# Performance work log

Measured on AMD Instinct MI355X. Metric: run time of the kernel, lower is better.

Reference implementation:

```python
import jax, jax.numpy as jnp
import numpy as np

UNITS = 768
OUT_STEPS = 64
INPUT_DIM = 96


def setup_inputs() -> dict:
    key = jax.random.key(0)
    ks = jax.random.split(key, 7)
    B, T = 2048, 24
    s_ih = 1.0 / np.sqrt(UNITS)
    inputs = jax.random.normal(ks[0], (B, T, INPUT_DIM), dtype=jnp.float32)
    # PyTorch LSTMCell params: weight_ih [4U, I], weight_hh [4U, U], biases [4U]
    W_ih = jax.random.uniform(ks[1], (4 * UNITS, INPUT_DIM), minval=-s_ih, maxval=s_ih, dtype=jnp.float32)
    W_hh = jax.random.uniform(ks[2], (4 * UNITS, UNITS), minval=-s_ih, maxval=s_ih, dtype=jnp.float32)
    b_ih = jax.random.uniform(ks[3], (4 * UNITS,), minval=-s_ih, maxval=s_ih, dtype=jnp.float32)
    b_hh = jax.random.uniform(ks[4], (4 * UNITS,), minval=-s_ih, maxval=s_ih, dtype=jnp.float32)
    # Dense: Linear(units, input_dim)
    s_d = 1.0 / np.sqrt(UNITS)
    W_d = jax.random.uniform(ks[5], (INPUT_DIM, UNITS), minval=-s_d, maxval=s_d, dtype=jnp.float32)
    b_d = jax.random.uniform(ks[6], (INPUT_DIM,), minval=-s_d, maxval=s_d, dtype=jnp.float32)
    return {"inputs": inputs, "W_ih": W_ih, "W_hh": W_hh, "b_ih": b_ih, "b_hh": b_hh, "W_d": W_d, "b_d": b_d}


def _lstm_cell(x, h, c, W_ih, W_hh, b_ih, b_hh):
    # gates: [B, 4U], PyTorch gate order i, f, g, o
    gates = x @ W_ih.T + b_ih + h @ W_hh.T + b_hh
    i, f, g, o = jnp.split(gates, 4, axis=-1)
    i = jax.nn.sigmoid(i)
    f = jax.nn.sigmoid(f)
    g = jnp.tanh(g)
    o = jax.nn.sigmoid(o)
    c_new = f * c + i * g
    h_new = o * jnp.tanh(c_new)
    return h_new, c_new


def reference(inputs, W_ih, W_hh, b_ih, b_hh, W_d, b_d):
    B = inputs.shape[0]
    h0 = jnp.zeros((B, UNITS), dtype=inputs.dtype)
    c0 = jnp.zeros((B, UNITS), dtype=inputs.dtype)
    # warmup: feed last timestep
    x0 = inputs[:, -1, :]
    h, c = _lstm_cell(x0, h0, c0, W_ih, W_hh, b_ih, b_hh)
    pred0 = h @ W_d.T + b_d

    def step(carry, _):
        pred, h, c = carry
        h2, c2 = _lstm_cell(pred, h, c, W_ih, W_hh, b_ih, b_hh)
        pred2 = h2 @ W_d.T + b_d
        return (pred2, h2, c2), pred2

    _, preds_rest = jax.lax.scan(step, (pred0, h, c), None, length=OUT_STEPS - 1)
    # preds_rest: [out_steps-1, B, I] -> stack with pred0 along time axis 1
    preds = jnp.concatenate([pred0[None], preds_rest], axis=0)  # [out_steps, B, I]
    return jnp.transpose(preds, (1, 0, 2))  # [B, out_steps, I]
```

## Files before the change

kernel.cpp:

```cpp
#include <hip/hip_runtime.h>
#include <hip/hip_bf16.h>
#include <stdint.h>

typedef __hip_bfloat16 bf16_t;
typedef __attribute__((ext_vector_type(4))) float f32x4;
typedef __attribute__((ext_vector_type(8))) short s16x8;

#define UNITS 768
#define NCOLS 3072
#define NPRED 96
#define MROWS 2048

__device__ __forceinline__ float sigf(float x) {
    return __builtin_amdgcn_rcpf(1.f + __expf(-x));
}
__device__ __forceinline__ float tanh_fast(float x) {
    return 1.f - 2.f * __builtin_amdgcn_rcpf(1.f + __expf(2.f * x));
}


__global__ void prep_b0(const float* __restrict__ W_ih, bf16_t* __restrict__ B0T) {
    int idx = blockIdx.x * 256 + threadIdx.x;
    if (idx >= NCOLS * 96) return;
    int c = idx / 96, k = idx % 96;
    int u = ((c >> 6) << 4) + (c & 15);
    int g = (c >> 4) & 3;
    B0T[idx] = (bf16_t)W_ih[(g * UNITS + u) * 96 + k];
}

__global__ void prep_x0(const float* __restrict__ inputs, bf16_t* __restrict__ x0) {
    int idx = blockIdx.x * 256 + threadIdx.x;
    int j = idx & 7;
    int l = (idx >> 3) & 63;
    int fg = idx >> 9;
    int kf = fg % 3;
    int mf = fg / 3;
    int m = mf * 16 + (l & 15);
    int k = kf * 32 + (l >> 4) * 8 + j;
    x0[idx] = (bf16_t)inputs[(m * 24 + 23) * 96 + k];
}

__global__ void prep_bias(const float* __restrict__ b_ih, const float* __restrict__ b_hh,
                          const float* __restrict__ W_ih, const float* __restrict__ b_d,
                          float* __restrict__ b0_r, float* __restrict__ beff_r) {
    int c = blockIdx.x * 256 + threadIdx.x;
    if (c >= NCOLS) return;
    int u = ((c >> 6) << 4) + (c & 15);
    int g = (c >> 4) & 3;
    int r = g * UNITS + u;
    float v = b_ih[r] + b_hh[r];
    float acc = 0.f;
    for (int j = 0; j < 96; ++j) acc += W_ih[r * 96 + j] * b_d[j];
    b0_r[c] = v;
    beff_r[c] = v + acc;
}

__global__ void prep_beff2(const float* __restrict__ W_hh, const float* __restrict__ W_ih,
                           const float* __restrict__ W_d, bf16_t* __restrict__ BeffT) {
    __shared__ float sWih[64][96];
    __shared__ float sWd[96][64];
    const int c0 = blockIdx.x * 64, k0 = blockIdx.y * 64;
    const int tid = threadIdx.x;
    for (int i = tid; i < 64 * 96; i += 256) {
        int cc = i / 96, j = i % 96;
        int c = c0 + cc;
        int u = ((c >> 6) << 4) + (c & 15);
        int g = (c >> 4) & 3;
        sWih[cc][j] = W_ih[(g * UNITS + u) * 96 + j];
    }
    for (int i = tid; i < 96 * 64; i += 256) {
        int j = i / 64, kk = i % 64;
        sWd[j][kk] = W_d[j * UNITS + k0 + kk];
    }
    __syncthreads();
    const int kk = tid & 63;
    const int cc0 = (tid >> 6) * 16;
    for (int cc = cc0; cc < cc0 + 16; ++cc) {
        float acc = 0.f;
#pragma unroll 12
        for (int j = 0; j < 96; ++j) acc += sWih[cc][j] * sWd[j][kk];
        int c = c0 + cc;
        int u = ((c >> 6) << 4) + (c & 15);
        int g = (c >> 4) & 3;
        int r = g * UNITS + u;
        BeffT[(size_t)c * UNITS + k0 + kk] = (bf16_t)(W_hh[(size_t)r * UNITS + k0 + kk] + acc);
    }
}

__global__ void prep_wdt(const float* __restrict__ W_d, bf16_t* __restrict__ BeffT) {
    int idx = blockIdx.x * 256 + threadIdx.x;
    int c = idx / UNITS, k = idx % UNITS;
    float v = (c < NPRED) ? W_d[c * UNITS + k] : 0.f;
    BeffT[(size_t)(NCOLS + c) * UNITS + k] = (bf16_t)v;
}

__global__ void prep_swz(const bf16_t* __restrict__ src, bf16_t* __restrict__ dst,
                         int Knk, int K, int total) {
    int idx = blockIdx.x * 256 + threadIdx.x;
    if (idx >= total) return;
    int j = idx & 7;
    int l = (idx >> 3) & 63;
    int fg = idx >> 9;
    int f = fg & 3;
    int rest = fg >> 2;
    int kf = rest % Knk;
    int nw = rest / Knk;
    int c = (nw >> 1) * 128 + (nw & 1) * 64 + f * 16 + (l & 15);
    int k = kf * 32 + (l >> 4) * 8 + j;
    dst[idx] = src[(size_t)c * K + k];
}

__global__ __launch_bounds__(256, 2)
void step_kernel(const bf16_t* __restrict__ A,
                 const bf16_t* __restrict__ B,
                 const float* __restrict__ bias_r,
                 const float* __restrict__ b_d,
                 float* __restrict__ c_state,
                 bf16_t* __restrict__ h_out,
                 float* __restrict__ out,
                 int Knk, int nt_off, int t, int is_first)
{
    const int tid = threadIdx.x;
    const int wave = tid >> 6;
    const int lane = tid & 63;
    const int wr = wave >> 1, wc = wave & 1;
    const int l15 = lane & 15, l4 = lane >> 4;

    const int per = gridDim.x >> 3;
    const int g = (blockIdx.x & 7) * per + (blockIdx.x >> 3);
    const int nt = nt_off + (g >> 4);
    const int mt = g & 15;
    const int n0 = nt * 128;
    const bool is_pred = (nt >= 24);

    const bf16_t* Ab[4];
#pragma unroll
    for (int i = 0; i < 4; ++i)
        Ab[i] = A + ((size_t)((mt * 8 + wr * 4 + i) * Knk) * 64 + lane) * 8;
    const bf16_t* Bb[4];
#pragma unroll
    for (int f = 0; f < 4; ++f)
        Bb[f] = B + ((size_t)((nt * 2 + wc) * Knk * 4 + f) * 64 + lane) * 8;

    const int u = nt * 32 + wc * 16 + l15;
    const int slot = nt * 16 + mt;
    float* cbase = c_state + (((size_t)slot * 4 + wave) * 64 + lane) * 16;
    f32x4 cold4[4];
    float bi[4];
#pragma unroll
    for (int q = 0; q < 4; ++q) cold4[q] = f32x4{0.f, 0.f, 0.f, 0.f};
    if (!is_pred) {
        if (!is_first) {
#pragma unroll
            for (int q = 0; q < 4; ++q) cold4[q] = *(const f32x4*)(cbase + q * 4);
        }
#pragma unroll
        for (int f = 0; f < 4; ++f) bi[f] = bias_r[n0 + wc * 64 + f * 16 + l15];
    } else {
#pragma unroll
        for (int f = 0; f < 4; ++f) {
            int j = wc * 64 + f * 16 + l15;
            bi[f] = (j < NPRED) ? b_d[j] : 0.f;
        }
    }

    f32x4 acc[4][4];
#pragma unroll
    for (int i = 0; i < 4; ++i)
#pragma unroll
        for (int j = 0; j < 4; ++j) acc[i][j] = f32x4{0.f, 0.f, 0.f, 0.f};

    s16x8 afr[3][4], bfr[3][4];
    const int nk = Knk;

#define LOADK(BUF, KT) do {                                                          \
        _Pragma("unroll")                                                            \
        for (int _i = 0; _i < 4; ++_i)                                               \
            afr[BUF][_i] = *(const s16x8*)(Ab[_i] + (size_t)(KT) * 512);             \
        _Pragma("unroll")                                                            \
        for (int _f = 0; _f < 4; ++_f)                                               \
            bfr[BUF][_f] = *(const s16x8*)(Bb[_f] + (size_t)(KT) * 2048);            \
    } while (0)
#define MF(BUF) do {                                                                 \
        _Pragma("unroll")                                                            \
        for (int _i = 0; _i < 4; ++_i)                                               \
            _Pragma("unroll")                                                        \
            for (int _j = 0; _j < 4; ++_j)                                           \
                acc[_i][_j] = __builtin_amdgcn_mfma_f32_16x16x32_bf16(               \
                    afr[BUF][_i], bfr[BUF][_j], acc[_i][_j], 0, 0, 0);               \
    } while (0)

    LOADK(0, 0);
    LOADK(1, 1);
    const int nk3 = nk / 3;
    for (int b3 = 0; b3 < nk3; ++b3) {
        const int kt = b3 * 3;
        if (kt + 2 < nk) LOADK(2, kt + 2);
        MF(0);
        if (kt + 3 < nk) LOADK(0, kt + 3);
        MF(1);
        if (kt + 4 < nk) LOADK(1, kt + 4);
        MF(2);
    }
#undef LOADK
#undef MF

    if (!is_pred) {
        const int kq = wc * 2 + (l15 >> 3);
        const int jj = l15 & 7;
        f32x4 cnew4[4];
#pragma unroll
        for (int i = 0; i < 4; ++i) {
            const int mf = mt * 8 + wr * 4 + i;
            bf16_t* hb = h_out + (size_t)(mf * 24 + nt) * 512;
#pragma unroll
            for (int r = 0; r < 4; ++r) {
                float gi = acc[i][0][r] + bi[0];
                float gf = acc[i][1][r] + bi[1];
                float gg = acc[i][2][r] + bi[2];
                float go = acc[i][3][r] + bi[3];
                float si = sigf(gi);
                float sf = sigf(gf);
                float tg = tanh_fast(gg);
                float so = sigf(go);
                float cn = sf * cold4[i][r] + si * tg;
                cnew4[i][r] = cn;
                int lp = (l4 * 4 + r) | (kq << 4);
                hb[lp * 8 + jj] = (bf16_t)(so * tanh_fast(cn));
            }
        }
#pragma unroll
        for (int q = 0; q < 4; ++q) *(f32x4*)(cbase + q * 4) = cnew4[q];
    } else {
#pragma unroll
        for (int f = 0; f < 4; ++f) {
            int j = wc * 64 + f * 16 + l15;
            if (j < NPRED) {
#pragma unroll
                for (int i = 0; i < 4; ++i)
#pragma unroll
                    for (int r = 0; r < 4; ++r) {
                        int row = mt * 128 + wr * 64 + i * 16 + l4 * 4 + r;
                        out[((size_t)row * 64 + (t - 1)) * NPRED + j] = acc[i][f][r] + bi[f];
                    }
            }
        }
    }
}

extern "C" void kernel_launch(void* const* d_in, const int* in_sizes, int n_in,
                              void* d_out, int out_size, void* d_ws, size_t ws_size,
                              hipStream_t stream)
{
    const float* inputs = (const float*)d_in[0];
    const float* W_ih   = (const float*)d_in[1];
    const float* W_hh   = (const float*)d_in[2];
    const float* b_ih   = (const float*)d_in[3];
    const float* b_hh   = (const float*)d_in[4];
    const float* W_d    = (const float*)d_in[5];
    const float* b_d    = (const float*)d_in[6];
    float* out = (float*)d_out;

    char* ws = (char*)d_ws;
    size_t off = 0;
    auto alloc = [&](size_t bytes) -> char* {
        char* p = ws + off;
        off = (off + bytes + 255) & ~(size_t)255;
        return p;
    };
    bf16_t* B0T   = (bf16_t*)alloc((size_t)NCOLS * 96 * 2);
    bf16_t* B0s   = (bf16_t*)alloc((size_t)NCOLS * 96 * 2);
    bf16_t* BeffT = (bf16_t*)alloc((size_t)3200 * UNITS * 2);
    bf16_t* Bs    = (bf16_t*)alloc((size_t)3200 * UNITS * 2);
    bf16_t* x0s   = (bf16_t*)alloc((size_t)MROWS * 96 * 2);
    bf16_t* h0    = (bf16_t*)alloc((size_t)MROWS * UNITS * 2);
    bf16_t* h1    = (bf16_t*)alloc((size_t)MROWS * UNITS * 2);
    float*  cst   = (float*)alloc((size_t)384 * 4 * 64 * 16 * 4);
    float*  b0r   = (float*)alloc(NCOLS * 4);
    float*  beffr = (float*)alloc(NCOLS * 4);

    prep_b0   <<<(NCOLS * 96 + 255) / 256, 256, 0, stream>>>(W_ih, B0T);
    prep_swz  <<<(NCOLS * 96 + 255) / 256, 256, 0, stream>>>(B0T, B0s, 3, 96, NCOLS * 96);
    prep_x0   <<<(MROWS * 96) / 256, 256, 0, stream>>>(inputs, x0s);
    prep_bias <<<(NCOLS + 255) / 256, 256, 0, stream>>>(b_ih, b_hh, W_ih, b_d, b0r, beffr);
    prep_beff2<<<dim3(48, 12), 256, 0, stream>>>(W_hh, W_ih, W_d, BeffT);
    prep_wdt  <<<(128 * UNITS) / 256, 256, 0, stream>>>(W_d, BeffT);
    prep_swz  <<<(3200 * UNITS + 255) / 256, 256, 0, stream>>>(BeffT, Bs, 24, UNITS, 3200 * UNITS);

    bf16_t* h[2] = {h0, h1};

    step_kernel<<<384, 256, 0, stream>>>(x0s, B0s, b0r, b_d, cst, h[1], out, 3, 0, 0, 1);
    for (int n = 1; n < 64; ++n)
        step_kernel<<<400, 256, 0, stream>>>(h[n & 1], Bs, beffr, b_d, cst,
                                             h[(n + 1) & 1], out, 24, 0, n, 0);
    step_kernel<<<16, 256, 0, stream>>>(h[0], Bs, beffr, b_d, cst, h[1], out,
                                        24, 24, 64, 0);
    (void)ws_size; (void)in_sizes; (void)n_in; (void)out_size;
}
```

Baseline: 1.347 ms.

## Replace per-step launches with persistent LSTM kernel using LDS-resident weights

Replaces the 65 per-timestep launches with one persistent kernel of 200 blocks. Each block keeps its 64-column weight slice in shared memory for all steps, keeps the cell state in registers, and synchronises with the other blocks of its row group through atomic counters in global memory. This removes launch overhead, repeated weight reloads from global memory, and cell-state round trips. In exchange it relies on all 200 blocks being co-resident and adds a spin barrier with a timeout escape after every step.

```diff
diff --git a/kernel.cpp b/kernel.cpp
--- a/kernel.cpp
+++ b/kernel.cpp
@@ -110,77 +110,108 @@
     dst[idx] = src[(size_t)c * K + k];
 }
 
-__global__ __launch_bounds__(256, 2)
-void step_kernel(const bf16_t* __restrict__ A,
-                 const bf16_t* __restrict__ B,
-                 const float* __restrict__ bias_r,
-                 const float* __restrict__ b_d,
-                 float* __restrict__ c_state,
-                 bf16_t* __restrict__ h_out,
-                 float* __restrict__ out,
-                 int Knk, int nt_off, int t, int is_first)
+__global__ void zero_ctr(int* __restrict__ c) {
+    c[threadIdx.x] = 0;
+}
+
+__global__ __launch_bounds__(512, 2)
+void lstm_persist(const bf16_t* __restrict__ x0s,
+                  const bf16_t* __restrict__ B0s,
+                  const bf16_t* __restrict__ Bs,
+                  const float* __restrict__ b0r,
+                  const float* __restrict__ beffr,
+                  const float* __restrict__ b_d,
+                  bf16_t* __restrict__ h0,
+                  bf16_t* __restrict__ h1,
+                  float* __restrict__ out,
+                  int* __restrict__ ctr)
 {
+    __shared__ __align__(16) bf16_t smem[24 * 4 * 512];
+
     const int tid = threadIdx.x;
-    const int wave = tid >> 6;
+    const int wr   = tid >> 6;
     const int lane = tid & 63;
-    const int wr = wave >> 1, wc = wave & 1;
     const int l15 = lane & 15, l4 = lane >> 4;
 
-    const int per = gridDim.x >> 3;
-    const int g = (blockIdx.x & 7) * per + (blockIdx.x >> 3);
-    const int nt = nt_off + (g >> 4);
-    const int mt = g & 15;
-    const int n0 = nt * 128;
-    const bool is_pred = (nt >= 24);
-
-    const bf16_t* Ab[4];
-#pragma unroll
-    for (int i = 0; i < 4; ++i)
-        Ab[i] = A + ((size_t)((mt * 8 + wr * 4 + i) * Knk) * 64 + lane) * 8;
-    const bf16_t* Bb[4];
+    const int bid  = blockIdx.x;
+    const int xcd  = bid & 7;
+    const int ii   = bid >> 3;
+    const int mt   = xcd >> 1;
+    const int nt64 = (xcd & 1) * 25 + ii;
+    const bool is_pred = (nt64 >= 48);
+    const int nt  = nt64 >> 1;
+    const int wcb = nt64 & 1;
+
+    {
+        const f32x4* src = (const f32x4*)(Bs + (size_t)nt64 * 49152);
+        f32x4* dst = (f32x4*)smem;
+        for (int i = tid; i < 6144; i += 512) dst[i] = src[i];
+    }
+
+    int aoffh[4], aoff0[4];
+#pragma unroll
+    for (int i = 0; i < 4; ++i) {
+        int mf = mt * 32 + wr * 4 + i;
+        aoffh[i] = (mf * 24) * 512 + lane * 8;
+        aoff0[i] = (mf * 3) * 512 + lane * 8;
+    }
+    int boff0[4];
 #pragma unroll
     for (int f = 0; f < 4; ++f)
-        Bb[f] = B + ((size_t)((nt * 2 + wc) * Knk * 4 + f) * 64 + lane) * 8;
-
-    const int u = nt * 32 + wc * 16 + l15;
-    const int slot = nt * 16 + mt;
-    float* cbase = c_state + (((size_t)slot * 4 + wave) * 64 + lane) * 16;
-    f32x4 cold4[4];
-    float bi[4];
-#pragma unroll
-    for (int q = 0; q < 4; ++q) cold4[q] = f32x4{0.f, 0.f, 0.f, 0.f};
+        boff0[f] = ((nt64 * 12 + f) * 64 + lane) * 8;
+
+    float bi0[4], biS[4];
     if (!is_pred) {
-        if (!is_first) {
-#pragma unroll
-            for (int q = 0; q < 4; ++q) cold4[q] = *(const f32x4*)(cbase + q * 4);
+#pragma unroll
+        for (int f = 0; f < 4; ++f) {
+            int idx = nt * 128 + wcb * 64 + f * 16 + l15;
+            bi0[f] = b0r[idx];
+            biS[f] = beffr[idx];
         }
-#pragma unroll
-        for (int f = 0; f < 4; ++f) bi[f] = bias_r[n0 + wc * 64 + f * 16 + l15];
     } else {
 #pragma unroll
         for (int f = 0; f < 4; ++f) {
-            int j = wc * 64 + f * 16 + l15;
-            bi[f] = (j < NPRED) ? b_d[j] : 0.f;
+            int j = wcb * 64 + f * 16 + l15;
+            biS[f] = (j < NPRED) ? b_d[j] : 0.f;
+            bi0[f] = 0.f;
         }
     }
 
+    const int kq = wcb * 2 + (l15 >> 3);
+    const int jj = l15 & 7;
+
+    f32x4 creg[4];
+#pragma unroll
+    for (int i = 0; i < 4; ++i) creg[i] = f32x4{0.f, 0.f, 0.f, 0.f};
+
+    int* cbase = ctr + mt * 64;
+
     f32x4 acc[4][4];
-#pragma unroll
-    for (int i = 0; i < 4; ++i)
-#pragma unroll
-        for (int j = 0; j < 4; ++j) acc[i][j] = f32x4{0.f, 0.f, 0.f, 0.f};
-
-    s16x8 afr[3][4], bfr[3][4];
-    const int nk = Knk;
-
-#define LOADK(BUF, KT) do {                                                          \
+
+#define ZACC() do {                                                                  \
+        _Pragma("unroll") for (int _i = 0; _i < 4; ++_i)                             \
+        _Pragma("unroll") for (int _j = 0; _j < 4; ++_j)                             \
+            acc[_i][_j] = f32x4{0.f, 0.f, 0.f, 0.f};                                 \
+    } while (0)
+
+#define LOADK_H(BUF, KT) do {                                                        \
         _Pragma("unroll")                                                            \
         for (int _i = 0; _i < 4; ++_i)                                               \
-            afr[BUF][_i] = *(const s16x8*)(Ab[_i] + (size_t)(KT) * 512);             \
+            afr[BUF][_i] = *(const s16x8*)(hA + aoffh[_i] + (size_t)(KT) * 512);     \
         _Pragma("unroll")                                                            \
         for (int _f = 0; _f < 4; ++_f)                                               \
-            bfr[BUF][_f] = *(const s16x8*)(Bb[_f] + (size_t)(KT) * 2048);            \
-    } while (0)
+            bfr[BUF][_f] = *(const s16x8*)(smem + ((KT) * 4 + _f) * 512 + lane * 8); \
+    } while (0)
+
+#define LOADK_0(BUF, KT) do {                                                        \
+        _Pragma("unroll")                                                            \
+        for (int _i = 0; _i < 4; ++_i)                                               \
+            afr[BUF][_i] = *(const s16x8*)(x0s + aoff0[_i] + (size_t)(KT) * 512);    \
+        _Pragma("unroll")                                                            \
+        for (int _f = 0; _f < 4; ++_f)                                               \
+            bfr[BUF][_f] = *(const s16x8*)(B0s + boff0[_f] + (size_t)(KT) * 2048);   \
+    } while (0)
+
 #define MF(BUF) do {                                                                 \
         _Pragma("unroll")                                                            \
         for (int _i = 0; _i < 4; ++_i)                                               \
@@ -190,62 +221,112 @@
                     afr[BUF][_i], bfr[BUF][_j], acc[_i][_j], 0, 0, 0);               \
     } while (0)
 
-    LOADK(0, 0);
-    LOADK(1, 1);
-    const int nk3 = nk / 3;
-    for (int b3 = 0; b3 < nk3; ++b3) {
-        const int kt = b3 * 3;
-        if (kt + 2 < nk) LOADK(2, kt + 2);
-        MF(0);
-        if (kt + 3 < nk) LOADK(0, kt + 3);
-        MF(1);
-        if (kt + 4 < nk) LOADK(1, kt + 4);
-        MF(2);
-    }
-#undef LOADK
+#define RUN3(NK, LOADK) do {                                                         \
+        s16x8 afr[3][4], bfr[3][4];                                                  \
+        LOADK(0, 0); LOADK(1, 1);                                                    \
+        const int _nk3 = (NK) / 3;                                                   \
+        for (int _b3 = 0; _b3 < _nk3; ++_b3) {                                       \
+            const int _kt = _b3 * 3;                                                 \
+            if (_kt + 2 < (NK)) LOADK(2, _kt + 2);                                   \
+            MF(0);                                                                   \
+            if (_kt + 3 < (NK)) LOADK(0, _kt + 3);                                   \
+            MF(1);                                                                   \
+            if (_kt + 4 < (NK)) LOADK(1, _kt + 4);                                   \
+            MF(2);                                                                   \
+        }                                                                            \
+    } while (0)
+
+#define GATE_EPI(HW, BI) do {                                                        \
+        _Pragma("unroll")                                                            \
+        for (int _i = 0; _i < 4; ++_i) {                                             \
+            const int _mf = mt * 32 + wr * 4 + _i;                                   \
+            bf16_t* _hb = (HW) + (size_t)(_mf * 24 + nt) * 512;                      \
+            _Pragma("unroll")                                                        \
+            for (int _r = 0; _r < 4; ++_r) {                                         \
+                float _gi = acc[_i][0][_r] + (BI)[0];                                \
+                float _gf = acc[_i][1][_r] + (BI)[1];                                \
+                float _gg = acc[_i][2][_r] + (BI)[2];                                \
+                float _go = acc[_i][3][_r] + (BI)[3];                                \
+                float _si = sigf(_gi);                                               \
+                float _sf = sigf(_gf);                                               \
+                float _tg = tanh_fast(_gg);                                          \
+                float _so = sigf(_go);                                               \
+                float _cn = _sf * creg[_i][_r] + _si * _tg;                          \
+                creg[_i][_r] = _cn;                                                  \
+                int _lp = (l4 * 4 + _r) | (kq << 4);                                 \
+                _hb[_lp * 8 + jj] = (bf16_t)(_so * tanh_fast(_cn));                  \
+            }                                                                        \
+        }                                                                            \
+    } while (0)
+
+#define PRED_EPI(TCOL) do {                                                          \
+        _Pragma("unroll")                                                            \
+        for (int _f = 0; _f < 4; ++_f) {                                             \
+            int _j = wcb * 64 + _f * 16 + l15;                                       \
+            if (_j < NPRED) {                                                        \
+                _Pragma("unroll")                                                    \
+                for (int _i = 0; _i < 4; ++_i)                                       \
+                    _Pragma("unroll")                                                \
+                    for (int _r = 0; _r < 4; ++_r) {                                 \
+                        int _row = mt * 512 + wr * 64 + _i * 16 + l4 * 4 + _r;       \
+                        out[((size_t)_row * 64 + (TCOL)) * NPRED + _j] =             \
+                            acc[_i][_f][_r] + biS[_f];                               \
+                    }                                                                \
+            }                                                                        \
+        }                                                                            \
+    } while (0)
+
+    auto barrier_step = [&](int s) {
+        __syncthreads();
+        if (tid == 0) {
+            __threadfence();
+            __hip_atomic_fetch_add(cbase + s, 1, __ATOMIC_RELEASE,
+                                   __HIP_MEMORY_SCOPE_AGENT);
+            int it = 0;
+            while (__hip_atomic_load(cbase + s, __ATOMIC_ACQUIRE,
+                                     __HIP_MEMORY_SCOPE_AGENT) < 50) {
+                __builtin_amdgcn_s_sleep(2);
+                if (++it > (1 << 22)) break;
+            }
+            __threadfence();
+        }
+        __syncthreads();
+    };
+
+    if (!is_pred) {
+        ZACC();
+        RUN3(3, LOADK_0);
+        GATE_EPI(h1, bi0);
+    }
+    barrier_step(0);
+
+    for (int s = 1; s < 64; ++s) {
+        const bf16_t* hA = (s & 1) ? h1 : h0;
+        ZACC();
+        RUN3(24, LOADK_H);
+        if (!is_pred) {
+            bf16_t* hW = ((s + 1) & 1) ? h1 : h0;
+            GATE_EPI(hW, biS);
+        } else {
+            PRED_EPI(s - 1);
+        }
+        barrier_step(s);
+    }
+
+    if (is_pred) {
+        const bf16_t* hA = h0;
+        ZACC();
+        RUN3(24, LOADK_H);
+        PRED_EPI(63);
+    }
+
+#undef ZACC
+#undef LOADK_H
+#undef LOADK_0
 #undef MF
-
-    if (!is_pred) {
-        const int kq = wc * 2 + (l15 >> 3);
-        const int jj = l15 & 7;
-        f32x4 cnew4[4];
-#pragma unroll
-        for (int i = 0; i < 4; ++i) {
-            const int mf = mt * 8 + wr * 4 + i;
-            bf16_t* hb = h_out + (size_t)(mf * 24 + nt) * 512;
-#pragma unroll
-            for (int r = 0; r < 4; ++r) {
-                float gi = acc[i][0][r] + bi[0];
-                float gf = acc[i][1][r] + bi[1];
-                float gg = acc[i][2][r] + bi[2];
-                float go = acc[i][3][r] + bi[3];
-                float si = sigf(gi);
-                float sf = sigf(gf);
-                float tg = tanh_fast(gg);
-                float so = sigf(go);
-                float cn = sf * cold4[i][r] + si * tg;
-                cnew4[i][r] = cn;
-                int lp = (l4 * 4 + r) | (kq << 4);
-                hb[lp * 8 + jj] = (bf16_t)(so * tanh_fast(cn));
-            }
-        }
-#pragma unroll
-        for (int q = 0; q < 4; ++q) *(f32x4*)(cbase + q * 4) = cnew4[q];
-    } else {
-#pragma unroll
-        for (int f = 0; f < 4; ++f) {
-            int j = wc * 64 + f * 16 + l15;
-            if (j < NPRED) {
-#pragma unroll
-                for (int i = 0; i < 4; ++i)
-#pragma unroll
-                    for (int r = 0; r < 4; ++r) {
-                        int row = mt * 128 + wr * 64 + i * 16 + l4 * 4 + r;
-                        out[((size_t)row * 64 + (t - 1)) * NPRED + j] = acc[i][f][r] + bi[f];
-                    }
-            }
-        }
-    }
+#undef RUN3
+#undef GATE_EPI
+#undef PRED_EPI
 }
 
 extern "C" void kernel_launch(void* const* d_in, const int* in_sizes, int n_in,
@@ -275,9 +356,9 @@
     bf16_t* x0s   = (bf16_t*)alloc((size_t)MROWS * 96 * 2);
     bf16_t* h0    = (bf16_t*)alloc((size_t)MROWS * UNITS * 2);
     bf16_t* h1    = (bf16_t*)alloc((size_t)MROWS * UNITS * 2);
-    float*  cst   = (float*)alloc((size_t)384 * 4 * 64 * 16 * 4);
     float*  b0r   = (float*)alloc(NCOLS * 4);
     float*  beffr = (float*)alloc(NCOLS * 4);
+    int*    ctr   = (int*)alloc(256 * 4);
 
     prep_b0   <<<(NCOLS * 96 + 255) / 256, 256, 0, stream>>>(W_ih, B0T);
     prep_swz  <<<(NCOLS * 96 + 255) / 256, 256, 0, stream>>>(B0T, B0s, 3, 96, NCOLS * 96);
@@ -286,14 +367,10 @@
     prep_beff2<<<dim3(48, 12), 256, 0, stream>>>(W_hh, W_ih, W_d, BeffT);
     prep_wdt  <<<(128 * UNITS) / 256, 256, 0, stream>>>(W_d, BeffT);
     prep_swz  <<<(3200 * UNITS + 255) / 256, 256, 0, stream>>>(BeffT, Bs, 24, UNITS, 3200 * UNITS);
-
-    bf16_t* h[2] = {h0, h1};
-
-    step_kernel<<<384, 256, 0, stream>>>(x0s, B0s, b0r, b_d, cst, h[1], out, 3, 0, 0, 1);
-    for (int n = 1; n < 64; ++n)
-        step_kernel<<<400, 256, 0, stream>>>(h[n & 1], Bs, beffr, b_d, cst,
-                                             h[(n + 1) & 1], out, 24, 0, n, 0);
-    step_kernel<<<16, 256, 0, stream>>>(h[0], Bs, beffr, b_d, cst, h[1], out,
-                                        24, 24, 64, 0);
+    zero_ctr  <<<1, 256, 0, stream>>>(ctr);
+
+    lstm_persist<<<200, 512, 0, stream>>>(x0s, B0s, Bs, b0r, beffr, b_d,
+                                          h0, h1, out, ctr);
+
     (void)ws_size; (void)in_sizes; (void)n_in; (void)out_size;
 }
```

Result: slower. 1.924 ms (+42.8%).
